# Performance work log

Measured on AMD Instinct MI355X. Metric: run time of the kernel, lower is better.

Reference implementation:

```python
import jax, jax.numpy as jnp
import numpy as np

B, S, E, P = 4, 2048, 1024, 4096

def setup_inputs() -> dict:
    key = jax.random.key(0)
    kx, kk, kv = jax.random.split(key, 3)
    x = jax.random.normal(kx, (B, S, E), dtype=jnp.float32)
    K = jax.random.normal(kk, (P, E), dtype=jnp.float32)
    V = jax.random.normal(kv, (P, E), dtype=jnp.float32)
    return {"x": x, "K": K, "V": V}

def reference(x, K, V):
    # scores: [B, S, P] = x @ K^T scaled by 1/sqrt(E)
    scale = jnp.asarray(x.shape[-1], x.dtype) ** -0.5
    scores = jnp.einsum('bse,pe->bsp', x, K) * scale
    attn = jax.nn.softmax(scores, axis=-1)
    # output: [B, S, E] = attn @ V
    return jnp.einsum('bsp,pe->bse', attn, V)
```

## Files before the change

### kernel.cpp

```cpp
#include <hip/hip_runtime.h>
#include <hip/hip_bf16.h>

typedef __attribute__((ext_vector_type(8))) short bf16x8;
typedef __attribute__((ext_vector_type(4))) float f32x4;
typedef __attribute__((ext_vector_type(8))) unsigned short u16x8;

__device__ __forceinline__ unsigned short f2bf(float f) {
  union { float f; unsigned u; } c; c.f = f;
  unsigned u = c.u;
  u = (u + 0x7FFFu + ((u >> 16) & 1u)) >> 16;
  return (unsigned short)u;
}

__device__ __forceinline__ void gld_lds16(const void* g, void* l) {
  __builtin_amdgcn_global_load_lds(
      (__attribute__((address_space(1))) unsigned int*)g,
      (__attribute__((address_space(3))) unsigned int*)l,
      16, 0, 0);
}

__global__ void cvt_all(const float* __restrict__ x, unsigned short* __restrict__ x16,
                        const float* __restrict__ Kw, unsigned short* __restrict__ K16,
                        const float* __restrict__ V, unsigned short* __restrict__ Vt,
                        float* __restrict__ lsum) {
  const int b = blockIdx.x;
  if (b < 32) lsum[b * 256 + threadIdx.x] = 0.f;

  if (b < 6144) {
    const float* in;
    unsigned short* out;
    int i;
    if (b < 4096) {
      in = x; out = x16; i = (b * 256 + threadIdx.x) * 8;
    } else {
      in = Kw; out = K16; i = ((b - 4096) * 256 + threadIdx.x) * 8;
    }
    const float4* p = (const float4*)(in + i);
    float4 a = p[0], bb = p[1];
    u16x8 r;
    r[0] = f2bf(a.x); r[1] = f2bf(a.y); r[2] = f2bf(a.z); r[3] = f2bf(a.w);
    r[4] = f2bf(bb.x); r[5] = f2bf(bb.y); r[6] = f2bf(bb.z); r[7] = f2bf(bb.w);
    *(u16x8*)(out + i) = r;
  } else {
    __shared__ unsigned short t[64][65];
    const int tile = b - 6144;
    const int p0 = (tile & 63) * 64;
    const int e0 = (tile >> 6) * 64;
    const int tx = threadIdx.x & 63;
    const int ty = threadIdx.x >> 6;
#pragma unroll
    for (int i = 0; i < 16; ++i) {
      int p = ty + i * 4;
      t[p][tx] = f2bf(V[(size_t)(p0 + p) * 1024 + e0 + tx]);
    }
    __syncthreads();
#pragma unroll
    for (int i = 0; i < 16; ++i) {
      int e = ty + i * 4;
      Vt[(size_t)(e0 + e) * 4096 + p0 + tx] = t[tx][e];
    }
  }
}

template <int EPI>
__global__ __launch_bounds__(256) void gemm_nt(
    const unsigned short* __restrict__ A, const unsigned short* __restrict__ B,
    int M, int N, int Kd,
    unsigned short* __restrict__ Pout, float* __restrict__ lsum,
    float* __restrict__ Cout, const float* __restrict__ lin, float scale) {
  __shared__ __align__(16) unsigned short sA[128 * 64];
  __shared__ __align__(16) unsigned short sB[128 * 64];

  const int tid = threadIdx.x;
  const int lane = tid & 63;
  const int w = tid >> 6;
  const int wm = w >> 1;
  const int wn = w & 1;

  int row0, col0;
  if constexpr (EPI == 0) {
    row0 = blockIdx.y * 128;
    col0 = blockIdx.x * 128;
  } else {
    int bid = blockIdx.x;
    row0 = (((bid >> 6) << 3) | (bid & 7)) * 128;
    col0 = ((bid >> 3) & 7) * 128;
  }

  f32x4 acc[4][4] = {};

  const unsigned short* pA[4];
  const unsigned short* pB[4];
  char* ldsA[4];
  char* ldsB[4];
#pragma unroll
  for (int j = 0; j < 4; ++j) {
    int c = j * 256 + tid;
    int r = c >> 3;
    int cs = (c & 7) ^ (r & 7);
    pA[j] = A + (size_t)(row0 + r) * Kd + cs * 8;
    pB[j] = B + (size_t)(col0 + r) * Kd + cs * 8;
    int off = (j * 256 + (w << 6)) * 16;
    ldsA[j] = (char*)sA + off;
    ldsB[j] = (char*)sB + off;
  }

  const int q = lane >> 4;
  const int ml = lane & 15;
  const char* fA[2];
  const char* fB[2];
#pragma unroll
  for (int ks = 0; ks < 2; ++ks) {
    int cc = (ks * 4 + q) ^ (ml & 7);
    fA[ks] = (const char*)sA + (wm * 64 + ml) * 128 + cc * 16;
    fB[ks] = (const char*)sB + (wn * 64 + ml) * 128 + cc * 16;
  }

  const int kIters = Kd >> 6;
  for (int it = 0; it < kIters; ++it) {
    __syncthreads();
#pragma unroll
    for (int j = 0; j < 4; ++j) {
      gld_lds16(pA[j], ldsA[j]);
      gld_lds16(pB[j], ldsB[j]);
      pA[j] += 64;
      pB[j] += 64;
    }
    __syncthreads();

#pragma unroll
    for (int ks = 0; ks < 2; ++ks) {
      bf16x8 af[4], bfr[4];
#pragma unroll
      for (int mi = 0; mi < 4; ++mi) af[mi] = *(const bf16x8*)(fA[ks] + mi * 2048);
#pragma unroll
      for (int ni = 0; ni < 4; ++ni) bfr[ni] = *(const bf16x8*)(fB[ks] + ni * 2048);
#pragma unroll
      for (int mi = 0; mi < 4; ++mi)
#pragma unroll
        for (int ni = 0; ni < 4; ++ni)
          acc[mi][ni] = __builtin_amdgcn_mfma_f32_16x16x32_bf16(
              af[mi], bfr[ni], acc[mi][ni], 0, 0, 0);
    }
  }

  if constexpr (EPI == 0) {
#pragma unroll
    for (int mi = 0; mi < 4; ++mi) {
#pragma unroll
      for (int j = 0; j < 4; ++j) {
        int gr = row0 + wm * 64 + mi * 16 + q * 4 + j;
        float rsum = 0.f;
#pragma unroll
        for (int ni = 0; ni < 4; ++ni) {
          int gc = col0 + wn * 64 + ni * 16 + ml;
          float p = exp2f(acc[mi][ni][j] * scale);
          rsum += p;
          Pout[(size_t)gr * N + gc] = f2bf(p);
        }
        rsum += __shfl_xor(rsum, 1);
        rsum += __shfl_xor(rsum, 2);
        rsum += __shfl_xor(rsum, 4);
        rsum += __shfl_xor(rsum, 8);
        if (ml == 0) atomicAdd(&lsum[gr], rsum);
      }
    }
  } else {
#pragma unroll
    for (int mi = 0; mi < 4; ++mi) {
#pragma unroll
      for (int j = 0; j < 4; ++j) {
        int gr = row0 + wm * 64 + mi * 16 + q * 4 + j;
        float rl = 1.0f / lin[gr];
#pragma unroll
        for (int ni = 0; ni < 4; ++ni) {
          int gc = col0 + wn * 64 + ni * 16 + ml;
          Cout[(size_t)gr * N + gc] = acc[mi][ni][j] * rl;
        }
      }
    }
  }
}

extern "C" void kernel_launch(void* const* d_in, const int* in_sizes, int n_in,
                              void* d_out, int out_size, void* d_ws,
                              size_t ws_size, hipStream_t stream) {
  const float* x = (const float*)d_in[0];
  const float* Kw = (const float*)d_in[1];
  const float* Vw = (const float*)d_in[2];
  float* out = (float*)d_out;
  char* ws = (char*)d_ws;

  unsigned short* x16  = (unsigned short*)(ws);
  unsigned short* K16  = (unsigned short*)(ws + (16u << 20));
  unsigned short* V16t = (unsigned short*)(ws + (24u << 20));
  float*          lsum = (float*)(ws + (32u << 20));
  unsigned short* P16  = (unsigned short*)(ws + (33u << 20));

  cvt_all<<<7168, 256, 0, stream>>>(x, x16, Kw, K16, Vw, V16t, lsum);

  gemm_nt<0><<<dim3(32, 64), 256, 0, stream>>>(
      x16, K16, 8192, 4096, 1024, P16, lsum, nullptr, nullptr,
      0.03125f * 1.44269504088896340736f);
  gemm_nt<1><<<512, 256, 0, stream>>>(
      P16, V16t, 8192, 1024, 4096, nullptr, nullptr, out, lsum, 1.0f);
}
```

Before: 268.4 us.

## Fuse conversion and both GEMMs into one cooperative persistent kernel

Replaces the three kernel launches with a single cooperative kernel of 512 blocks that performs the bf16 conversion, the scores GEMM with exp epilogue, and the output GEMM. Grid-wide syncs separate the phases. The aim is to remove launch gaps and tail effects between kernels. In exchange, each block processes 4 tiles serially in the first GEMM and 512 blocks may underfill the GPU. The host now also queries device attributes and occupancy on every call, and falls back to the original three launches if cooperative launch is unavailable.

```diff
diff --git a/kernel.cpp b/kernel.cpp
--- a/kernel.cpp
+++ b/kernel.cpp
@@ -1,5 +1,8 @@
 #include <hip/hip_runtime.h>
 #include <hip/hip_bf16.h>
+#include <hip/hip_cooperative_groups.h>
+
+namespace cg = cooperative_groups;
 
 typedef __attribute__((ext_vector_type(8))) short bf16x8;
 typedef __attribute__((ext_vector_type(4))) float f32x4;
@@ -19,73 +22,60 @@
       16, 0, 0);
 }
 
-__global__ void cvt_all(const float* __restrict__ x, unsigned short* __restrict__ x16,
-                        const float* __restrict__ Kw, unsigned short* __restrict__ K16,
-                        const float* __restrict__ V, unsigned short* __restrict__ Vt,
-                        float* __restrict__ lsum) {
-  const int b = blockIdx.x;
-  if (b < 32) lsum[b * 256 + threadIdx.x] = 0.f;
-
-  if (b < 6144) {
+__device__ __forceinline__ void cvt_job(
+    int j, int tid, unsigned short* smem,
+    const float* __restrict__ x, unsigned short* __restrict__ x16,
+    const float* __restrict__ Kw, unsigned short* __restrict__ K16,
+    const float* __restrict__ Vw, unsigned short* __restrict__ V16t) {
+  if (j < 6144) {
     const float* in;
-    unsigned short* out;
+    unsigned short* o;
     int i;
-    if (b < 4096) {
-      in = x; out = x16; i = (b * 256 + threadIdx.x) * 8;
+    if (j < 4096) {
+      in = x; o = x16; i = (j * 256 + tid) * 8;
     } else {
-      in = Kw; out = K16; i = ((b - 4096) * 256 + threadIdx.x) * 8;
+      in = Kw; o = K16; i = ((j - 4096) * 256 + tid) * 8;
     }
     const float4* p = (const float4*)(in + i);
     float4 a = p[0], bb = p[1];
     u16x8 r;
     r[0] = f2bf(a.x); r[1] = f2bf(a.y); r[2] = f2bf(a.z); r[3] = f2bf(a.w);
     r[4] = f2bf(bb.x); r[5] = f2bf(bb.y); r[6] = f2bf(bb.z); r[7] = f2bf(bb.w);
-    *(u16x8*)(out + i) = r;
+    *(u16x8*)(o + i) = r;
   } else {
-    __shared__ unsigned short t[64][65];
-    const int tile = b - 6144;
+    unsigned short(*t)[65] = (unsigned short(*)[65])smem;
+    __syncthreads();
+    const int tile = j - 6144;
     const int p0 = (tile & 63) * 64;
     const int e0 = (tile >> 6) * 64;
-    const int tx = threadIdx.x & 63;
-    const int ty = threadIdx.x >> 6;
+    const int tx = tid & 63;
+    const int ty = tid >> 6;
 #pragma unroll
     for (int i = 0; i < 16; ++i) {
       int p = ty + i * 4;
-      t[p][tx] = f2bf(V[(size_t)(p0 + p) * 1024 + e0 + tx]);
+      t[p][tx] = f2bf(Vw[(size_t)(p0 + p) * 1024 + e0 + tx]);
     }
     __syncthreads();
 #pragma unroll
     for (int i = 0; i < 16; ++i) {
       int e = ty + i * 4;
-      Vt[(size_t)(e0 + e) * 4096 + p0 + tx] = t[tx][e];
+      V16t[(size_t)(e0 + e) * 4096 + p0 + tx] = t[tx][e];
     }
   }
 }
 
 template <int EPI>
-__global__ __launch_bounds__(256) void gemm_nt(
+__device__ __forceinline__ void gemm_tile(
     const unsigned short* __restrict__ A, const unsigned short* __restrict__ B,
-    int M, int N, int Kd,
+    int row0, int col0, int Kd, int N,
+    unsigned short* sA, unsigned short* sB,
     unsigned short* __restrict__ Pout, float* __restrict__ lsum,
     float* __restrict__ Cout, const float* __restrict__ lin, float scale) {
-  __shared__ __align__(16) unsigned short sA[128 * 64];
-  __shared__ __align__(16) unsigned short sB[128 * 64];
-
   const int tid = threadIdx.x;
   const int lane = tid & 63;
   const int w = tid >> 6;
   const int wm = w >> 1;
   const int wn = w & 1;
-
-  int row0, col0;
-  if constexpr (EPI == 0) {
-    row0 = blockIdx.y * 128;
-    col0 = blockIdx.x * 128;
-  } else {
-    int bid = blockIdx.x;
-    row0 = (((bid >> 6) << 3) | (bid & 7)) * 128;
-    col0 = ((bid >> 3) & 7) * 128;
-  }
 
   f32x4 acc[4][4] = {};
 
@@ -127,7 +117,6 @@
       pB[j] += 64;
     }
     __syncthreads();
-
 #pragma unroll
     for (int ks = 0; ks < 2; ++ks) {
       bf16x8 af[4], bfr[4];
@@ -182,6 +171,78 @@
   }
 }
 
+__global__ __launch_bounds__(256) void fused_all(
+    const float* __restrict__ x, const float* __restrict__ Kw,
+    const float* __restrict__ Vw,
+    unsigned short* __restrict__ x16, unsigned short* __restrict__ K16,
+    unsigned short* __restrict__ V16t, unsigned short* __restrict__ P16,
+    float* __restrict__ lsum, float* __restrict__ out) {
+  __shared__ __align__(16) unsigned short smem[2 * 128 * 64];
+  unsigned short* sA = smem;
+  unsigned short* sB = smem + 128 * 64;
+
+  const int b = blockIdx.x;
+  const int tid = threadIdx.x;
+
+  if (b < 32) lsum[b * 256 + tid] = 0.f;
+  for (int j = b; j < 7168; j += 512)
+    cvt_job(j, tid, smem, x, x16, Kw, K16, Vw, V16t);
+
+  __threadfence();
+  cg::this_grid().sync();
+
+  {
+    const int m = b >> 3;
+    const float sc = 0.03125f * 1.44269504088896340736f;
+#pragma unroll 1
+    for (int t = 0; t < 4; ++t) {
+      const int n = (b & 7) * 4 + t;
+      gemm_tile<0>(x16, K16, m * 128, n * 128, 1024, 4096, sA, sB,
+                   P16, lsum, nullptr, nullptr, sc);
+    }
+  }
+
+  __threadfence();
+  cg::this_grid().sync();
+
+  {
+    const int m = ((b >> 6) << 3) | (b & 7);
+    const int n = (b >> 3) & 7;
+    gemm_tile<1>(P16, V16t, m * 128, n * 128, 4096, 1024, sA, sB,
+                 nullptr, nullptr, out, lsum, 1.0f);
+  }
+}
+
+__global__ void cvt_all_k(const float* __restrict__ x, unsigned short* __restrict__ x16,
+                          const float* __restrict__ Kw, unsigned short* __restrict__ K16,
+                          const float* __restrict__ Vw, unsigned short* __restrict__ V16t,
+                          float* __restrict__ lsum) {
+  __shared__ __align__(16) unsigned short smem[64 * 65];
+  if (blockIdx.x < 32) lsum[blockIdx.x * 256 + threadIdx.x] = 0.f;
+  cvt_job(blockIdx.x, threadIdx.x, smem, x, x16, Kw, K16, Vw, V16t);
+}
+
+__global__ __launch_bounds__(256) void gemm1_k(
+    const unsigned short* __restrict__ A, const unsigned short* __restrict__ B,
+    unsigned short* __restrict__ P, float* __restrict__ lsum, float scale) {
+  __shared__ __align__(16) unsigned short sA[128 * 64];
+  __shared__ __align__(16) unsigned short sB[128 * 64];
+  gemm_tile<0>(A, B, blockIdx.y * 128, blockIdx.x * 128, 1024, 4096, sA, sB,
+               P, lsum, nullptr, nullptr, scale);
+}
+
+__global__ __launch_bounds__(256) void gemm2_k(
+    const unsigned short* __restrict__ A, const unsigned short* __restrict__ B,
+    float* __restrict__ out, const float* __restrict__ lsum) {
+  __shared__ __align__(16) unsigned short sA[128 * 64];
+  __shared__ __align__(16) unsigned short sB[128 * 64];
+  const int bid = blockIdx.x;
+  const int row0 = (((bid >> 6) << 3) | (bid & 7)) * 128;
+  const int col0 = ((bid >> 3) & 7) * 128;
+  gemm_tile<1>(A, B, row0, col0, 4096, 1024, sA, sB,
+               nullptr, nullptr, out, lsum, 1.0f);
+}
+
 extern "C" void kernel_launch(void* const* d_in, const int* in_sizes, int n_in,
                               void* d_out, int out_size, void* d_ws,
                               size_t ws_size, hipStream_t stream) {
@@ -197,11 +258,29 @@
   float*          lsum = (float*)(ws + (32u << 20));
   unsigned short* P16  = (unsigned short*)(ws + (33u << 20));
 
-  cvt_all<<<7168, 256, 0, stream>>>(x, x16, Kw, K16, Vw, V16t, lsum);
-
-  gemm_nt<0><<<dim3(32, 64), 256, 0, stream>>>(
-      x16, K16, 8192, 4096, 1024, P16, lsum, nullptr, nullptr,
-      0.03125f * 1.44269504088896340736f);
-  gemm_nt<1><<<512, 256, 0, stream>>>(
-      P16, V16t, 8192, 1024, 4096, nullptr, nullptr, out, lsum, 1.0f);
-}
+  const float sc = 0.03125f * 1.44269504088896340736f;
+
+  int dev = 0;
+  (void)hipGetDevice(&dev);
+  int coop_attr = 0;
+  (void)hipDeviceGetAttribute(&coop_attr, hipDeviceAttributeCooperativeLaunch, dev);
+  int maxb = 0;
+  (void)hipOccupancyMaxActiveBlocksPerMultiprocessor(
+      &maxb, reinterpret_cast<const void*>(fused_all), 256, 0);
+
+  bool done = false;
+  if (coop_attr != 0 && maxb >= 2) {
+    void* args[] = {(void*)&x,    (void*)&Kw,   (void*)&Vw,
+                    (void*)&x16,  (void*)&K16,  (void*)&V16t,
+                    (void*)&P16,  (void*)&lsum, (void*)&out};
+    hipError_t e = hipLaunchCooperativeKernel((void*)fused_all, dim3(512),
+                                              dim3(256), args, 0, stream);
+    done = (e == hipSuccess);
+  }
+
+  if (!done) {
+    cvt_all_k<<<7168, 256, 0, stream>>>(x, x16, Kw, K16, Vw, V16t, lsum);
+    gemm1_k<<<dim3(32, 64), 256, 0, stream>>>(x16, K16, P16, lsum, sc);
+    gemm2_k<<<512, 256, 0, stream>>>(P16, V16t, out, lsum);
+  }
+}
```

Result: no change. 273.1 us (+1.8%).

## Fuse both GEMMs into one persistent-order launch with per-row-block completion counters

Applied to the files above, without the earlier changes.

Merges the score GEMM and the PV GEMM into a single launch. Blocks 0..2047 compute the exp'd score tiles and signal a per-128-row counter. Blocks 2048+ spin-wait on that counter before running the output GEMM for their row block. This removes the kernel boundary and lets PV work on finished row blocks overlap with the tail of the first GEMM. In exchange it adds atomic signalling and spin-waiting, and it relies on block dispatch order to avoid deadlock. It also sets launch_bounds to 4 waves per SIMD.

```diff
diff --git a/kernel.cpp b/kernel.cpp
--- a/kernel.cpp
+++ b/kernel.cpp
@@ -19,73 +19,59 @@
       16, 0, 0);
 }
 
-__global__ void cvt_all(const float* __restrict__ x, unsigned short* __restrict__ x16,
-                        const float* __restrict__ Kw, unsigned short* __restrict__ K16,
-                        const float* __restrict__ V, unsigned short* __restrict__ Vt,
-                        float* __restrict__ lsum) {
-  const int b = blockIdx.x;
-  if (b < 32) lsum[b * 256 + threadIdx.x] = 0.f;
-
-  if (b < 6144) {
+__device__ __forceinline__ void cvt_job(
+    int j, int tid, unsigned short* smem,
+    const float* __restrict__ x, unsigned short* __restrict__ x16,
+    const float* __restrict__ Kw, unsigned short* __restrict__ K16,
+    const float* __restrict__ Vw, unsigned short* __restrict__ V16t) {
+  if (j < 6144) {
     const float* in;
-    unsigned short* out;
+    unsigned short* o;
     int i;
-    if (b < 4096) {
-      in = x; out = x16; i = (b * 256 + threadIdx.x) * 8;
+    if (j < 4096) {
+      in = x; o = x16; i = (j * 256 + tid) * 8;
     } else {
-      in = Kw; out = K16; i = ((b - 4096) * 256 + threadIdx.x) * 8;
+      in = Kw; o = K16; i = ((j - 4096) * 256 + tid) * 8;
     }
     const float4* p = (const float4*)(in + i);
     float4 a = p[0], bb = p[1];
     u16x8 r;
     r[0] = f2bf(a.x); r[1] = f2bf(a.y); r[2] = f2bf(a.z); r[3] = f2bf(a.w);
     r[4] = f2bf(bb.x); r[5] = f2bf(bb.y); r[6] = f2bf(bb.z); r[7] = f2bf(bb.w);
-    *(u16x8*)(out + i) = r;
+    *(u16x8*)(o + i) = r;
   } else {
-    __shared__ unsigned short t[64][65];
-    const int tile = b - 6144;
+    unsigned short(*t)[65] = (unsigned short(*)[65])smem;
+    const int tile = j - 6144;
     const int p0 = (tile & 63) * 64;
     const int e0 = (tile >> 6) * 64;
-    const int tx = threadIdx.x & 63;
-    const int ty = threadIdx.x >> 6;
+    const int tx = tid & 63;
+    const int ty = tid >> 6;
 #pragma unroll
     for (int i = 0; i < 16; ++i) {
       int p = ty + i * 4;
-      t[p][tx] = f2bf(V[(size_t)(p0 + p) * 1024 + e0 + tx]);
+      t[p][tx] = f2bf(Vw[(size_t)(p0 + p) * 1024 + e0 + tx]);
     }
     __syncthreads();
 #pragma unroll
     for (int i = 0; i < 16; ++i) {
       int e = ty + i * 4;
-      Vt[(size_t)(e0 + e) * 4096 + p0 + tx] = t[tx][e];
+      V16t[(size_t)(e0 + e) * 4096 + p0 + tx] = t[tx][e];
     }
   }
 }
 
 template <int EPI>
-__global__ __launch_bounds__(256) void gemm_nt(
+__device__ __forceinline__ void gemm_tile(
     const unsigned short* __restrict__ A, const unsigned short* __restrict__ B,
-    int M, int N, int Kd,
+    int row0, int col0, int Kd, int N,
+    unsigned short* sA, unsigned short* sB,
     unsigned short* __restrict__ Pout, float* __restrict__ lsum,
     float* __restrict__ Cout, const float* __restrict__ lin, float scale) {
-  __shared__ __align__(16) unsigned short sA[128 * 64];
-  __shared__ __align__(16) unsigned short sB[128 * 64];
-
   const int tid = threadIdx.x;
   const int lane = tid & 63;
   const int w = tid >> 6;
   const int wm = w >> 1;
   const int wn = w & 1;
-
-  int row0, col0;
-  if constexpr (EPI == 0) {
-    row0 = blockIdx.y * 128;
-    col0 = blockIdx.x * 128;
-  } else {
-    int bid = blockIdx.x;
-    row0 = (((bid >> 6) << 3) | (bid & 7)) * 128;
-    col0 = ((bid >> 3) & 7) * 128;
-  }
 
   f32x4 acc[4][4] = {};
 
@@ -127,7 +113,6 @@
       pB[j] += 64;
     }
     __syncthreads();
-
 #pragma unroll
     for (int ks = 0; ks < 2; ++ks) {
       bf16x8 af[4], bfr[4];
@@ -182,6 +167,50 @@
   }
 }
 
+__global__ void cvt_all_k(const float* __restrict__ x, unsigned short* __restrict__ x16,
+                          const float* __restrict__ Kw, unsigned short* __restrict__ K16,
+                          const float* __restrict__ Vw, unsigned short* __restrict__ V16t,
+                          float* __restrict__ lsum, unsigned int* __restrict__ ctr) {
+  __shared__ __align__(16) unsigned short smem[64 * 65];
+  if (blockIdx.x < 32) lsum[blockIdx.x * 256 + threadIdx.x] = 0.f;
+  if (blockIdx.x == 32 && threadIdx.x < 64) ctr[threadIdx.x] = 0u;
+  cvt_job(blockIdx.x, threadIdx.x, smem, x, x16, Kw, K16, Vw, V16t);
+}
+
+__global__ __launch_bounds__(256, 4) void gemm_fused(
+    const unsigned short* __restrict__ x16, const unsigned short* __restrict__ K16,
+    const unsigned short* __restrict__ V16t, unsigned short* __restrict__ P16,
+    float* __restrict__ lsum, float* __restrict__ out,
+    unsigned int* __restrict__ ctr) {
+  __shared__ __align__(16) unsigned short sA[128 * 64];
+  __shared__ __align__(16) unsigned short sB[128 * 64];
+  const int b = blockIdx.x;
+
+  if (b < 2048) {
+    const int m = b >> 5;
+    const int n = b & 31;
+    const float sc = 0.03125f * 1.44269504088896340736f;
+    gemm_tile<0>(x16, K16, m * 128, n * 128, 1024, 4096, sA, sB,
+                 P16, lsum, nullptr, nullptr, sc);
+    __syncthreads();
+    if (threadIdx.x == 0)
+      __hip_atomic_fetch_add(&ctr[m], 1u, __ATOMIC_RELEASE,
+                             __HIP_MEMORY_SCOPE_AGENT);
+  } else {
+    const int b2 = b - 2048;
+    const int m = b2 >> 3;
+    const int n = b2 & 7;
+    if (threadIdx.x == 0) {
+      while (__hip_atomic_load(&ctr[m], __ATOMIC_ACQUIRE,
+                               __HIP_MEMORY_SCOPE_AGENT) < 32u)
+        __builtin_amdgcn_s_sleep(16);
+    }
+    __syncthreads();
+    gemm_tile<1>(P16, V16t, m * 128, n * 128, 4096, 1024, sA, sB,
+                 nullptr, nullptr, out, lsum, 1.0f);
+  }
+}
+
 extern "C" void kernel_launch(void* const* d_in, const int* in_sizes, int n_in,
                               void* d_out, int out_size, void* d_ws,
                               size_t ws_size, hipStream_t stream) {
@@ -195,13 +224,9 @@
   unsigned short* K16  = (unsigned short*)(ws + (16u << 20));
   unsigned short* V16t = (unsigned short*)(ws + (24u << 20));
   float*          lsum = (float*)(ws + (32u << 20));
+  unsigned int*   ctr  = (unsigned int*)(ws + (32u << 20) + 32768);
   unsigned short* P16  = (unsigned short*)(ws + (33u << 20));
 
-  cvt_all<<<7168, 256, 0, stream>>>(x, x16, Kw, K16, Vw, V16t, lsum);
-
-  gemm_nt<0><<<dim3(32, 64), 256, 0, stream>>>(
-      x16, K16, 8192, 4096, 1024, P16, lsum, nullptr, nullptr,
-      0.03125f * 1.44269504088896340736f);
-  gemm_nt<1><<<512, 256, 0, stream>>>(
-      P16, V16t, 8192, 1024, 4096, nullptr, nullptr, out, lsum, 1.0f);
-}
+  cvt_all_k<<<7168, 256, 0, stream>>>(x, x16, Kw, K16, Vw, V16t, lsum, ctr);
+  gemm_fused<<<2560, 256, 0, stream>>>(x16, K16, V16t, P16, lsum, out, ctr);
+}
```

After: 481.9 us. 1.8x slower.
